# Kernel optimization log

Measured on AMD Instinct MI355X. Metric: run time of the kernel, lower is better.

The kernel has to match this reference:

```python
import jax, jax.numpy as jnp
import numpy as np

NUM_EMB = 1024
EMB_DIM = 256
COMMITMENT_COST = 0.25


def setup_inputs() -> dict:
    key = jax.random.key(0)
    k1, k2 = jax.random.split(key)
    inp = jax.random.normal(k1, (64, EMB_DIM, 32, 32), dtype=jnp.float32)  # [B, C, H, W]
    emb_weight = jax.random.uniform(
        k2, (NUM_EMB, EMB_DIM), minval=-1.0 / NUM_EMB, maxval=1.0 / NUM_EMB, dtype=jnp.float32
    )
    return {"inp": inp, "emb_weight": emb_weight}


def reference(inp, emb_weight):
    sg = jax.lax.stop_gradient
    x = jnp.transpose(inp, (0, 2, 3, 1))              # [B, H, W, C]
    flat = x.reshape(-1, EMB_DIM)                      # [N, C]
    d = (jnp.sum(flat * flat, axis=1, keepdims=True)
         + jnp.sum(emb_weight * emb_weight, axis=1)
         - 2.0 * (flat @ emb_weight.T))
    idx = jnp.argmin(d, axis=1)                        # [N]
    encodings = jax.nn.one_hot(idx, NUM_EMB, dtype=jnp.float32)  # [N, K]
    e = emb_weight[idx].reshape(x.shape)               # [B, H, W, C]
    loss = jnp.mean((e - sg(x)) ** 2) + COMMITMENT_COST * jnp.mean((sg(e) - x) ** 2)
    e_ste = x + sg(e - x)                              # straight-through estimator
    avg_probs = jnp.mean(encodings, axis=0)
    perplexity = jnp.exp(-jnp.sum(avg_probs * jnp.log(avg_probs + 1e-10)))
    out = jnp.transpose(e_ste, (0, 3, 1, 2))           # back to [B, C, H, W]
    return loss, out, perplexity, encodings
```

## Files before the change

### kernel.cpp

```cpp
#include <hip/hip_runtime.h>
#include <hip/hip_bf16.h>
#include <math.h>
#include <float.h>

#define BB    64
#define CCH   256
#define KKE   1024
#define HWN   1024
#define NTOT  (BB*HWN)
#define OUT_ELE (BB*CCH*HWN)
#define LOSS_OFF 0
#define OUT_OFF  1
#define PERP_OFF (1 + OUT_ELE)
#define ENC_OFF  (2 + OUT_ELE)

#define WS_IDX    0
#define WS_ANORM  262144
#define WS_HIST   524288
#define WS_BNORM  528384
#define WS_MISC   532480
#define WS_LIST   536576
#define WS_EMBT   798720
#define WS_EHI    1847296
#define WS_ELO    2371584
#define WS_CD1    2895872
#define WS_CK1    4993024
#define WS_CD2    7090176

typedef __attribute__((ext_vector_type(4))) float f32x4;
typedef __attribute__((ext_vector_type(8))) short s16x8;

#define TAU 2e-4f

__device__ inline void merge_cand(float& d1, int& k1, float& d2,
                                  float od1, int ok1, float od2) {
    bool w = (od1 < d1) || (od1 == d1 && ok1 < k1);
    float loser_d1 = w ? d1 : od1;
    float winner_d2 = w ? od2 : d2;
    d2 = fminf(winner_d2, loser_d1);
    if (w) { d1 = od1; k1 = ok1; }
}

__global__ __launch_bounds__(256) void prep_kernel(const float* __restrict__ emb,
                                                   float* __restrict__ embT,
                                                   float* __restrict__ bnorm,
                                                   short* __restrict__ ehi,
                                                   short* __restrict__ elo,
                                                   unsigned int* __restrict__ hist,
                                                   float* __restrict__ misc) {
    const int k = blockIdx.x;
    const int t = threadIdx.x;
    float v = emb[k*CCH + t];
    embT[(size_t)t*KKE + k] = v;
    __hip_bfloat16 h = __float2bfloat16(v);
    float hf = __bfloat162float(h);
    __hip_bfloat16 l = __float2bfloat16(v - hf);
    size_t eoff = (size_t)(t >> 5)*32768 + (size_t)k*32 + (t & 31);
    ehi[eoff] = *(short*)&h;
    elo[eoff] = *(short*)&l;
    double sq = (double)v * (double)v;
    #pragma unroll
    for (int off = 32; off; off >>= 1) sq += __shfl_down(sq, off);
    __shared__ double wred[4];
    const int wave = t >> 6, lane = t & 63;
    if (lane == 0) wred[wave] = sq;
    __syncthreads();
    if (t == 0) bnorm[k] = (float)(wred[0] + wred[1] + wred[2] + wred[3]);
    if (blockIdx.x < 4) hist[blockIdx.x*256 + t] = 0u;
    if (blockIdx.x == 4 && t == 0) { misc[0] = 0.0f; ((int*)misc)[1] = 0; }
}

__global__ __launch_bounds__(256) void anorm_kernel(const float* __restrict__ inp,
                                                    float* __restrict__ anorm) {
    const int b  = blockIdx.y;
    const int hw = blockIdx.x * 256 + threadIdx.x;
    const float* p = inp + (size_t)b*CCH*HWN + hw;
    double s = 0.0;
    #pragma unroll 8
    for (int c = 0; c < CCH; ++c) {
        float v = p[(size_t)c*HWN];
        s += (double)v * (double)v;
    }
    anorm[b*HWN + hw] = (float)s;
}

__global__ __launch_bounds__(256, 3) void argmin_mfma(const float* __restrict__ inp,
                                                      const short* __restrict__ ehi,
                                                      const short* __restrict__ elo,
                                                      const float* __restrict__ anorm,
                                                      const float* __restrict__ bnorm,
                                                      float* __restrict__ cd1,
                                                      int* __restrict__ ck1,
                                                      float* __restrict__ cd2) {
    __shared__ short Ahi[128*40];
    __shared__ short Alo[128*40];
    __shared__ short Bhi[128*40];
    __shared__ short Blo[128*40];

    const int t    = threadIdx.x;
    const int w    = t >> 6;
    const int lane = t & 63;
    const int q    = lane >> 4;
    const int l15  = lane & 15;
    const int n0   = blockIdx.x * 128;
    const int k0   = blockIdx.y * 128;
    const int b    = n0 >> 10;
    const int hw0  = n0 & 1023;
    const float* gA = inp + (size_t)b*CCH*HWN + hw0;

    const int na = t & 127;
    const int ch = t >> 7;
    const int br = t >> 2;
    const int bc = (t & 3) * 8;

    f32x4 acc[2][8];
    #pragma unroll
    for (int i = 0; i < 2; ++i)
        #pragma unroll
        for (int j = 0; j < 8; ++j) acc[i][j] = (f32x4){0.f,0.f,0.f,0.f};

    for (int chunk = 0; chunk < 8; ++chunk) {
        const int c0 = chunk * 32;
        __syncthreads();
        float v[16];
        #pragma unroll
        for (int cc = 0; cc < 16; ++cc)
            v[cc] = gA[(size_t)(c0 + ch*16 + cc) * HWN + na];
        short hs[16], ls[16];
        #pragma unroll
        for (int cc = 0; cc < 16; ++cc) {
            __hip_bfloat16 h = __float2bfloat16(v[cc]);
            float hf = __bfloat162float(h);
            __hip_bfloat16 l = __float2bfloat16(v[cc] - hf);
            hs[cc] = *(short*)&h; ls[cc] = *(short*)&l;
        }
        *(s16x8*)&Ahi[na*40 + ch*16]     = *(s16x8*)&hs[0];
        *(s16x8*)&Ahi[na*40 + ch*16 + 8] = *(s16x8*)&hs[8];
        *(s16x8*)&Alo[na*40 + ch*16]     = *(s16x8*)&ls[0];
        *(s16x8*)&Alo[na*40 + ch*16 + 8] = *(s16x8*)&ls[8];
        {
            const size_t ebase = (size_t)chunk*32768 + (size_t)k0*32;
            *(s16x8*)&Bhi[br*40 + bc]        = *(const s16x8*)&ehi[ebase + t*8];
            *(s16x8*)&Bhi[(64+br)*40 + bc]   = *(const s16x8*)&ehi[ebase + 2048 + t*8];
            *(s16x8*)&Blo[br*40 + bc]        = *(const s16x8*)&elo[ebase + t*8];
            *(s16x8*)&Blo[(64+br)*40 + bc]   = *(const s16x8*)&elo[ebase + 2048 + t*8];
        }
        __syncthreads();
        s16x8 afh0 = *(s16x8*)&Ahi[(w*32 +      l15)*40 + q*8];
        s16x8 afh1 = *(s16x8*)&Ahi[(w*32 + 16 + l15)*40 + q*8];
        s16x8 afl0 = *(s16x8*)&Alo[(w*32 +      l15)*40 + q*8];
        s16x8 afl1 = *(s16x8*)&Alo[(w*32 + 16 + l15)*40 + q*8];
        #pragma unroll
        for (int ct = 0; ct < 8; ++ct) {
            s16x8 bh = *(s16x8*)&Bhi[(ct*16 + l15)*40 + q*8];
            s16x8 bl = *(s16x8*)&Blo[(ct*16 + l15)*40 + q*8];
            acc[0][ct] = __builtin_amdgcn_mfma_f32_16x16x32_bf16(afh0, bh, acc[0][ct], 0, 0, 0);
            acc[0][ct] = __builtin_amdgcn_mfma_f32_16x16x32_bf16(afh0, bl, acc[0][ct], 0, 0, 0);
            acc[0][ct] = __builtin_amdgcn_mfma_f32_16x16x32_bf16(afl0, bh, acc[0][ct], 0, 0, 0);
            acc[1][ct] = __builtin_amdgcn_mfma_f32_16x16x32_bf16(afh1, bh, acc[1][ct], 0, 0, 0);
            acc[1][ct] = __builtin_amdgcn_mfma_f32_16x16x32_bf16(afh1, bl, acc[1][ct], 0, 0, 0);
            acc[1][ct] = __builtin_amdgcn_mfma_f32_16x16x32_bf16(afl1, bh, acc[1][ct], 0, 0, 0);
        }
    }

    float bnv[8];
    #pragma unroll
    for (int ct = 0; ct < 8; ++ct) bnv[ct] = bnorm[k0 + ct*16 + l15];

    #pragma unroll
    for (int rg = 0; rg < 2; ++rg) {
        #pragma unroll
        for (int reg = 0; reg < 4; ++reg) {
            const int n = n0 + w*32 + rg*16 + q*4 + reg;
            const float a = anorm[n];
            float d1 = FLT_MAX, d2 = FLT_MAX; int k1 = 0;
            #pragma unroll
            for (int ct = 0; ct < 8; ++ct) {
                float s = a + bnv[ct];
                float d = s - 2.0f * acc[rg][ct][reg];
                int   k = k0 + ct*16 + l15;
                if (d < d1 || (d == d1 && k < k1)) { d2 = d1; d1 = d; k1 = k; }
                else d2 = fminf(d2, d);
            }
            #pragma unroll
            for (int off = 1; off < 16; off <<= 1) {
                float od1 = __shfl_xor(d1, off);
                int   ok1 = __shfl_xor(k1, off);
                float od2 = __shfl_xor(d2, off);
                merge_cand(d1, k1, d2, od1, ok1, od2);
            }
            if (l15 == 0) {
                const size_t o = (size_t)blockIdx.y*NTOT + n;
                cd1[o] = d1; ck1[o] = k1; cd2[o] = d2;
            }
        }
    }
}

__global__ __launch_bounds__(256) void reduce_kernel(const float* __restrict__ cd1,
                                                     const int* __restrict__ ck1,
                                                     const float* __restrict__ cd2,
                                                     int* __restrict__ idx,
                                                     int* __restrict__ list,
                                                     int* __restrict__ counter) {
    const int n = blockIdx.x*256 + threadIdx.x;
    float d1 = cd1[n]; int k1 = ck1[n]; float d2 = cd2[n];
    #pragma unroll
    for (int kb = 1; kb < 8; ++kb) {
        const size_t o = (size_t)kb*NTOT + n;
        merge_cand(d1, k1, d2, cd1[o], ck1[o], cd2[o]);
    }
    idx[n] = k1;
    if (d2 - d1 < TAU) {
        int p = atomicAdd(counter, 1);
        list[p] = n;
    }
}

__global__ __launch_bounds__(256) void rescore_kernel(const float* __restrict__ inp,
                                                      const float* __restrict__ embT,
                                                      const float* __restrict__ anorm,
                                                      const float* __restrict__ bnorm,
                                                      const int* __restrict__ list,
                                                      const int* __restrict__ counter,
                                                      int* __restrict__ idx) {
    __shared__ float xs[256];
    __shared__ float rd[256];
    __shared__ int   rk[256];
    const int t = threadIdx.x;
    const int cnt = *counter;
    for (int f = blockIdx.x; f < cnt; f += gridDim.x) {
        const int n = list[f];
        const int b = n >> 10, hw = n & 1023;
        __syncthreads();
        xs[t] = inp[(size_t)b*CCH*HWN + (size_t)t*HWN + hw];
        __syncthreads();
        float dot0 = 0.f, dot1 = 0.f, dot2 = 0.f, dot3 = 0.f;
        #pragma unroll 4
        for (int c = 0; c < CCH; ++c) {
            const float xc = xs[c];
            const float* row = embT + (size_t)c*KKE + t;
            dot0 += xc * row[0];
            dot1 += xc * row[256];
            dot2 += xc * row[512];
            dot3 += xc * row[768];
        }
        const float a = anorm[n];
        float bd = FLT_MAX; int bk = 0;
        float dots[4] = {dot0, dot1, dot2, dot3};
        #pragma unroll
        for (int kk = 0; kk < 4; ++kk) {
            const int k = kk*256 + t;
            float s = a + bnorm[k];
            float d = s - 2.0f * dots[kk];
            if (d < bd || (d == bd && k < bk)) { bd = d; bk = k; }
        }
        rd[t] = bd; rk[t] = bk;
        __syncthreads();
        for (int stride = 128; stride; stride >>= 1) {
            if (t < stride) {
                float od = rd[t+stride]; int ok = rk[t+stride];
                if (od < rd[t] || (od == rd[t] && ok < rk[t])) { rd[t] = od; rk[t] = ok; }
            }
            __syncthreads();
        }
        if (t == 0) idx[n] = rk[0];
    }
}

__global__ __launch_bounds__(256) void onehot_kernel(const int* __restrict__ idx,
                                                     float* __restrict__ enc,
                                                     unsigned int* __restrict__ hist) {
    const int t = threadIdx.x;
    const int j4 = t * 4;
    for (int r = 0; r < 16; ++r) {
        const int n = blockIdx.x*16 + r;
        const int k = idx[n];
        float2 v0 = {0.0f, 0.0f}, v1 = {0.0f, 0.0f};
        if (k == j4)     v0.x = 1.0f;
        if (k == j4 + 1) v0.y = 1.0f;
        if (k == j4 + 2) v1.x = 1.0f;
        if (k == j4 + 3) v1.y = 1.0f;
        float* row = enc + (size_t)n * KKE;
        *(float2*)&row[j4]     = v0;
        *(float2*)&row[j4 + 2] = v1;
        if (t == 0) atomicAdd(&hist[k], 1u);
    }
}

__global__ __launch_bounds__(256) void out_loss_kernel(const float* __restrict__ inp,
                                                       const float* __restrict__ embT,
                                                       const int* __restrict__ idx,
                                                       float* __restrict__ out,
                                                       float* __restrict__ lossacc) {
    const int t = threadIdx.x;
    const size_t stride = (size_t)gridDim.x * 256;
    float lsum = 0.0f;
    for (size_t m = (size_t)blockIdx.x * 256 + t; m < (size_t)OUT_ELE; m += stride) {
        int hw = (int)(m & 1023);
        int c  = (int)((m >> 10) & 255);
        int b  = (int)(m >> 18);
        int k  = idx[b*HWN + hw];
        float e = embT[(size_t)c*KKE + k];
        float x = inp[m];
        out[m] = e;
        float df = e - x;
        lsum += df * df;
    }
    #pragma unroll
    for (int off = 32; off; off >>= 1) lsum += __shfl_down(lsum, off);
    __shared__ float wred[4];
    const int wave = t >> 6, lane = t & 63;
    if (lane == 0) wred[wave] = lsum;
    __syncthreads();
    if (t == 0) atomicAdd(lossacc, wred[0] + wred[1] + wred[2] + wred[3]);
}

__global__ __launch_bounds__(1024) void final_kernel(const unsigned int* __restrict__ hist,
                                                     const float* __restrict__ lossacc,
                                                     float* __restrict__ d_out) {
    const int t = threadIdx.x;
    float p = (float)hist[t] * (1.0f / 65536.0f);
    float v = p * logf(p + 1e-10f);
    #pragma unroll
    for (int off = 32; off; off >>= 1) v += __shfl_down(v, off);
    __shared__ float wred[16];
    const int wave = t >> 6, lane = t & 63;
    if (lane == 0) wred[wave] = v;
    __syncthreads();
    if (t == 0) {
        float s = 0.0f;
        #pragma unroll
        for (int i = 0; i < 16; ++i) s += wred[i];
        d_out[PERP_OFF] = expf(-s);
        d_out[LOSS_OFF] = 1.25f * (*lossacc) * (1.0f / (float)OUT_ELE);
    }
}

extern "C" void kernel_launch(void* const* d_in, const int* in_sizes, int n_in,
                              void* d_out, int out_size, void* d_ws, size_t ws_size,
                              hipStream_t stream) {
    (void)in_sizes; (void)n_in; (void)out_size; (void)ws_size;
    const float* inp = (const float*)d_in[0];
    const float* emb = (const float*)d_in[1];
    float* out = (float*)d_out;
    char* ws = (char*)d_ws;
    int*          idx     = (int*)(ws + WS_IDX);
    float*        anorm   = (float*)(ws + WS_ANORM);
    unsigned int* hist    = (unsigned int*)(ws + WS_HIST);
    float*        bnorm   = (float*)(ws + WS_BNORM);
    float*        misc    = (float*)(ws + WS_MISC);
    int*          list    = (int*)(ws + WS_LIST);
    float*        embT    = (float*)(ws + WS_EMBT);
    short*        ehi     = (short*)(ws + WS_EHI);
    short*        elo     = (short*)(ws + WS_ELO);
    float*        cd1     = (float*)(ws + WS_CD1);
    int*          ck1     = (int*)(ws + WS_CK1);
    float*        cd2     = (float*)(ws + WS_CD2);
    int*          counter = ((int*)misc) + 1;

    prep_kernel<<<dim3(KKE), dim3(256), 0, stream>>>(emb, embT, bnorm, ehi, elo, hist, misc);
    anorm_kernel<<<dim3(4, BB), dim3(256), 0, stream>>>(inp, anorm);
    argmin_mfma<<<dim3(512, 8), dim3(256), 0, stream>>>(inp, ehi, elo, anorm, bnorm, cd1, ck1, cd2);
    reduce_kernel<<<dim3(256), dim3(256), 0, stream>>>(cd1, ck1, cd2, idx, list, counter);
    rescore_kernel<<<dim3(512), dim3(256), 0, stream>>>(inp, embT, anorm, bnorm, list, counter, idx);
    onehot_kernel<<<dim3(4096), dim3(256), 0, stream>>>(idx, out + ENC_OFF, hist);
    out_loss_kernel<<<dim3(4096), dim3(256), 0, stream>>>(inp, embT, idx, out + OUT_OFF, misc);
    final_kernel<<<dim3(1), dim3(1024), 0, stream>>>(hist, misc, out);
}
```

Measured before the change: 743.8 us.

## Pre-split inputs to bf16 hi/lo in swizzled layout and use direct global-to-LDS loads

A new pre-pass kernel converts the input activations once into bf16 hi/lo pairs, stored chunk-major with an XOR swizzle, and also computes row norms. The embedding split uses the same swizzle. The argmin GEMM kernel now fills shared memory with global_load_lds 16-byte transfers instead of loading fp32, converting and storing per tile, which removes redundant conversion work across the 8 K-blocks and avoids LDS bank conflicts without padding. The cost is a 64 MB workspace write and read of the split activations, plus reliance on the global_load_lds builtin.

```diff
diff --git a/kernel.cpp b/kernel.cpp
--- a/kernel.cpp
+++ b/kernel.cpp
@@ -26,11 +26,20 @@
 #define WS_CD1    2895872
 #define WS_CK1    4993024
 #define WS_CD2    7090176
+#define WS_AHI    9187328
+#define WS_ALO    42741760
 
 typedef __attribute__((ext_vector_type(4))) float f32x4;
 typedef __attribute__((ext_vector_type(8))) short s16x8;
 
 #define TAU 2e-4f
+
+__device__ __forceinline__ void gload16(const short* g, void* l) {
+    __builtin_amdgcn_global_load_lds(
+        (const __attribute__((address_space(1))) unsigned int*)g,
+        (__attribute__((address_space(3))) unsigned int*)l,
+        16, 0, 0);
+}
 
 __device__ inline void merge_cand(float& d1, int& k1, float& d2,
                                   float od1, int ok1, float od2) {
@@ -55,7 +64,9 @@
     __hip_bfloat16 h = __float2bfloat16(v);
     float hf = __bfloat162float(h);
     __hip_bfloat16 l = __float2bfloat16(v - hf);
-    size_t eoff = (size_t)(t >> 5)*32768 + (size_t)k*32 + (t & 31);
+    const int u  = (t & 31) >> 3;
+    const int sw = (k >> 1) & 3;
+    size_t eoff = (size_t)(t >> 5)*32768 + (size_t)k*32 + (size_t)((u ^ sw)*8 + (t & 7));
     ehi[eoff] = *(short*)&h;
     elo[eoff] = *(short*)&l;
     double sq = (double)v * (double)v;
@@ -70,21 +81,41 @@
     if (blockIdx.x == 4 && t == 0) { misc[0] = 0.0f; ((int*)misc)[1] = 0; }
 }
 
-__global__ __launch_bounds__(256) void anorm_kernel(const float* __restrict__ inp,
-                                                    float* __restrict__ anorm) {
+__global__ __launch_bounds__(256) void asplit_kernel(const float* __restrict__ inp,
+                                                     short* __restrict__ ahi,
+                                                     short* __restrict__ alo,
+                                                     float* __restrict__ anorm) {
+    const int t  = threadIdx.x;
     const int b  = blockIdx.y;
-    const int hw = blockIdx.x * 256 + threadIdx.x;
-    const float* p = inp + (size_t)b*CCH*HWN + hw;
+    const int hw = blockIdx.x * 256 + t;
+    const int n  = b * HWN + hw;
+    const float* src = inp + (size_t)b*CCH*HWN + hw;
+    const int sw = (n >> 1) & 3;
     double s = 0.0;
-    #pragma unroll 8
-    for (int c = 0; c < CCH; ++c) {
-        float v = p[(size_t)c*HWN];
-        s += (double)v * (double)v;
-    }
-    anorm[b*HWN + hw] = (float)s;
-}
-
-__global__ __launch_bounds__(256, 3) void argmin_mfma(const float* __restrict__ inp,
+    for (int chunk = 0; chunk < 8; ++chunk) {
+        s16x8 hs[4], ls[4];
+        #pragma unroll
+        for (int cc = 0; cc < 32; ++cc) {
+            float v = src[(size_t)(chunk*32 + cc)*HWN];
+            s += (double)v * (double)v;
+            __hip_bfloat16 h = __float2bfloat16(v);
+            float hf = __bfloat162float(h);
+            __hip_bfloat16 l = __float2bfloat16(v - hf);
+            hs[cc >> 3][cc & 7] = *(short*)&h;
+            ls[cc >> 3][cc & 7] = *(short*)&l;
+        }
+        const size_t obase = ((size_t)chunk*NTOT + (size_t)n) * 32;
+        #pragma unroll
+        for (int u = 0; u < 4; ++u) {
+            *(s16x8*)&ahi[obase + (size_t)((u ^ sw) * 8)] = hs[u];
+            *(s16x8*)&alo[obase + (size_t)((u ^ sw) * 8)] = ls[u];
+        }
+    }
+    anorm[n] = (float)s;
+}
+
+__global__ __launch_bounds__(256, 3) void argmin_mfma(const short* __restrict__ ahi,
+                                                      const short* __restrict__ alo,
                                                       const short* __restrict__ ehi,
                                                       const short* __restrict__ elo,
                                                       const float* __restrict__ anorm,
@@ -92,10 +123,7 @@
                                                       float* __restrict__ cd1,
                                                       int* __restrict__ ck1,
                                                       float* __restrict__ cd2) {
-    __shared__ short Ahi[128*40];
-    __shared__ short Alo[128*40];
-    __shared__ short Bhi[128*40];
-    __shared__ short Blo[128*40];
+    __shared__ short smem[4][4096];
 
     const int t    = threadIdx.x;
     const int w    = t >> 6;
@@ -104,14 +132,6 @@
     const int l15  = lane & 15;
     const int n0   = blockIdx.x * 128;
     const int k0   = blockIdx.y * 128;
-    const int b    = n0 >> 10;
-    const int hw0  = n0 & 1023;
-    const float* gA = inp + (size_t)b*CCH*HWN + hw0;
-
-    const int na = t & 127;
-    const int ch = t >> 7;
-    const int br = t >> 2;
-    const int bc = (t & 3) * 8;
 
     f32x4 acc[2][8];
     #pragma unroll
@@ -119,41 +139,40 @@
         #pragma unroll
         for (int j = 0; j < 8; ++j) acc[i][j] = (f32x4){0.f,0.f,0.f,0.f};
 
+    const int swu = (q ^ ((l15 >> 1) & 3)) << 4;
+    const int ra0 = (w*32 + l15)*64 + swu;
+
     for (int chunk = 0; chunk < 8; ++chunk) {
-        const int c0 = chunk * 32;
-        __syncthreads();
-        float v[16];
-        #pragma unroll
-        for (int cc = 0; cc < 16; ++cc)
-            v[cc] = gA[(size_t)(c0 + ch*16 + cc) * HWN + na];
-        short hs[16], ls[16];
-        #pragma unroll
-        for (int cc = 0; cc < 16; ++cc) {
-            __hip_bfloat16 h = __float2bfloat16(v[cc]);
-            float hf = __bfloat162float(h);
-            __hip_bfloat16 l = __float2bfloat16(v[cc] - hf);
-            hs[cc] = *(short*)&h; ls[cc] = *(short*)&l;
-        }
-        *(s16x8*)&Ahi[na*40 + ch*16]     = *(s16x8*)&hs[0];
-        *(s16x8*)&Ahi[na*40 + ch*16 + 8] = *(s16x8*)&hs[8];
-        *(s16x8*)&Alo[na*40 + ch*16]     = *(s16x8*)&ls[0];
-        *(s16x8*)&Alo[na*40 + ch*16 + 8] = *(s16x8*)&ls[8];
+        __syncthreads();
         {
-            const size_t ebase = (size_t)chunk*32768 + (size_t)k0*32;
-            *(s16x8*)&Bhi[br*40 + bc]        = *(const s16x8*)&ehi[ebase + t*8];
-            *(s16x8*)&Bhi[(64+br)*40 + bc]   = *(const s16x8*)&ehi[ebase + 2048 + t*8];
-            *(s16x8*)&Blo[br*40 + bc]        = *(const s16x8*)&elo[ebase + t*8];
-            *(s16x8*)&Blo[(64+br)*40 + bc]   = *(const s16x8*)&elo[ebase + 2048 + t*8];
-        }
-        __syncthreads();
-        s16x8 afh0 = *(s16x8*)&Ahi[(w*32 +      l15)*40 + q*8];
-        s16x8 afh1 = *(s16x8*)&Ahi[(w*32 + 16 + l15)*40 + q*8];
-        s16x8 afl0 = *(s16x8*)&Alo[(w*32 +      l15)*40 + q*8];
-        s16x8 afl1 = *(s16x8*)&Alo[(w*32 + 16 + l15)*40 + q*8];
+            const short* as = ahi + (size_t)chunk*2097152 + (size_t)n0*32;
+            const short* al = alo + (size_t)chunk*2097152 + (size_t)n0*32;
+            const short* bs = ehi + (size_t)chunk*32768  + (size_t)k0*32;
+            const short* bl = elo + (size_t)chunk*32768  + (size_t)k0*32;
+            #pragma unroll
+            for (int i = 0; i < 2; ++i) {
+                const size_t so = (size_t)i*2048 + (size_t)t*8;
+                const int    lo = i*4096 + w*1024;
+                gload16(as + so, (char*)&smem[0][0] + lo);
+                gload16(al + so, (char*)&smem[1][0] + lo);
+                gload16(bs + so, (char*)&smem[2][0] + lo);
+                gload16(bl + so, (char*)&smem[3][0] + lo);
+            }
+        }
+        __syncthreads();
+        const char* LAh = (const char*)&smem[0][0];
+        const char* LAl = (const char*)&smem[1][0];
+        const char* LBh = (const char*)&smem[2][0];
+        const char* LBl = (const char*)&smem[3][0];
+        s16x8 afh0 = *(const s16x8*)(LAh + ra0);
+        s16x8 afh1 = *(const s16x8*)(LAh + ra0 + 1024);
+        s16x8 afl0 = *(const s16x8*)(LAl + ra0);
+        s16x8 afl1 = *(const s16x8*)(LAl + ra0 + 1024);
         #pragma unroll
         for (int ct = 0; ct < 8; ++ct) {
-            s16x8 bh = *(s16x8*)&Bhi[(ct*16 + l15)*40 + q*8];
-            s16x8 bl = *(s16x8*)&Blo[(ct*16 + l15)*40 + q*8];
+            const int rb = (ct*16 + l15)*64 + swu;
+            s16x8 bh = *(const s16x8*)(LBh + rb);
+            s16x8 bl = *(const s16x8*)(LBl + rb);
             acc[0][ct] = __builtin_amdgcn_mfma_f32_16x16x32_bf16(afh0, bh, acc[0][ct], 0, 0, 0);
             acc[0][ct] = __builtin_amdgcn_mfma_f32_16x16x32_bf16(afh0, bl, acc[0][ct], 0, 0, 0);
             acc[0][ct] = __builtin_amdgcn_mfma_f32_16x16x32_bf16(afl0, bh, acc[0][ct], 0, 0, 0);
@@ -357,11 +376,13 @@
     float*        cd1     = (float*)(ws + WS_CD1);
     int*          ck1     = (int*)(ws + WS_CK1);
     float*        cd2     = (float*)(ws + WS_CD2);
+    short*        ahi     = (short*)(ws + WS_AHI);
+    short*        alo     = (short*)(ws + WS_ALO);
     int*          counter = ((int*)misc) + 1;
 
     prep_kernel<<<dim3(KKE), dim3(256), 0, stream>>>(emb, embT, bnorm, ehi, elo, hist, misc);
-    anorm_kernel<<<dim3(4, BB), dim3(256), 0, stream>>>(inp, anorm);
-    argmin_mfma<<<dim3(512, 8), dim3(256), 0, stream>>>(inp, ehi, elo, anorm, bnorm, cd1, ck1, cd2);
+    asplit_kernel<<<dim3(4, BB), dim3(256), 0, stream>>>(inp, ahi, alo, anorm);
+    argmin_mfma<<<dim3(512, 8), dim3(256), 0, stream>>>(ahi, alo, ehi, elo, anorm, bnorm, cd1, ck1, cd2);
     reduce_kernel<<<dim3(256), dim3(256), 0, stream>>>(cd1, ck1, cd2, idx, list, counter);
     rescore_kernel<<<dim3(512), dim3(256), 0, stream>>>(inp, embT, anorm, bnorm, list, counter, idx);
     onehot_kernel<<<dim3(4096), dim3(256), 0, stream>>>(idx, out + ENC_OFF, hist);
```

After: 742.3 us. No clear change (-0.2%).
